# Performance work log

Measured on AMD Instinct MI355X. Metric: run time of the kernel, lower is better.

## Reference

```python
import jax, jax.numpy as jnp
from jax import lax
import numpy as np

B, C, L, H, W = 2, 64, 16, 64, 64
K = 7
NG = 4  # GroupNorm groups (SpatialGroupNorm(4, channels))


def setup_inputs() -> dict:
    key = jax.random.key(0)
    ks = jax.random.split(key, 16)
    s = lambda i, shape, sc: jax.random.normal(ks[i], shape, jnp.float32) * sc
    return {
        "x": s(0, (B, C, L, H, W), 1.0),
        "dt": jax.random.uniform(ks[1], (B, L), jnp.float32, 0.1, 1.0),
        "W_sp": s(2, (C, C, K, K), 0.02),      # spatial 7x7 conv (OIHW)
        "W_dc": s(3, (C, C), 0.1),             # 1x1x1 depth conv
        "b_dc": jnp.zeros((C,), jnp.float32),
        "gn_g": jnp.ones((C,), jnp.float32),
        "gn_b": jnp.zeros((C,), jnp.float32),
        "W_in": s(4, (2 * C, C), 0.1),         # pw_conv_in 1x1 -> 2C (gated)
        "b_in": jnp.zeros((2 * C,), jnp.float32),
        "W_out": s(5, (C, C), 0.1),            # pw_conv_out 1x1
        "b_out": jnp.zeros((C,), jnp.float32),
        "nu_log": s(6, (C,), 0.5),             # LRU log decay rate
        "theta_log": s(7, (C,), 0.5),          # LRU log frequency
        "c_re": s(8, (C,), 0.5),               # LRU output mix (real)
        "c_im": s(9, (C,), 0.5),               # LRU output mix (imag)
        "d_skip": s(10, (C,), 0.5),            # LRU feedthrough
    }


def reference(x, dt, W_sp, W_dc, b_dc, gn_g, gn_b, W_in, b_in, W_out, b_out,
              nu_log, theta_log, c_re, c_im, d_skip):
    Bb, Cc, Ll, Hh, Ww = x.shape
    pad = W_sp.shape[-1] // 2
    # --- GatedConvBlock: FactorizedPeriodicConv3d (per-frame 2D conv) ---
    xf = x.transpose(0, 2, 1, 3, 4).reshape(Bb * Ll, Cc, Hh, Ww)  # [B*L,C,H,W]
    xp = jnp.pad(xf, ((0, 0), (0, 0), (0, 0), (pad, pad)), mode='wrap')    # circular W
    xp = jnp.pad(xp, ((0, 0), (0, 0), (pad, pad), (0, 0)), mode='edge')    # replicate H
    y = lax.conv_general_dilated(xp, W_sp, (1, 1), 'VALID',
                                 dimension_numbers=('NCHW', 'OIHW', 'NCHW'))
    y = jnp.einsum('nchw,oc->nohw', y, W_dc) + b_dc[None, :, None, None]   # depth 1x1x1
    # --- SpatialGroupNorm (per frame, 4 groups) ---
    g = y.reshape(Bb * Ll, NG, Cc // NG, Hh, Ww)
    mu = g.mean(axis=(2, 3, 4), keepdims=True)
    var = g.var(axis=(2, 3, 4), keepdims=True)
    y = ((g - mu) * lax.rsqrt(var + 1e-5)).reshape(Bb * Ll, Cc, Hh, Ww)
    y = y * gn_g[None, :, None, None] + gn_b[None, :, None, None]
    # --- gated pointwise convs + residual ---
    h = jnp.einsum('nchw,oc->nohw', y, W_in) + b_in[None, :, None, None]
    x1, x2 = jnp.split(h, 2, axis=1)
    z = x1 * jax.nn.sigmoid(x2)
    z = jnp.einsum('nchw,oc->nohw', z, W_out) + b_out[None, :, None, None]
    u = xf + z                                     # residual, [B*L,C,H,W]
    u = u.reshape(Bb, Ll, Cc, Hh, Ww).transpose(1, 0, 2, 3, 4)  # [L,B,C,H,W]
    # --- LRU: dt-dependent complex diagonal recurrence over L ---
    decay = jnp.exp(-jnp.exp(nu_log)[None, None, :] * dt[:, :, None])   # [B,L,C]
    phase = jnp.exp(theta_log)[None, None, :] * dt[:, :, None]          # [B,L,C]
    lam_re = (decay * jnp.cos(phase)).transpose(1, 0, 2)[..., None, None]  # [L,B,C,1,1]
    lam_im = (decay * jnp.sin(phase)).transpose(1, 0, 2)[..., None, None]
    gamma = jnp.sqrt(jnp.maximum(1.0 - decay ** 2, 1e-6)).transpose(1, 0, 2)[..., None, None]
    cr = c_re[None, :, None, None]
    ci = c_im[None, :, None, None]
    ds = d_skip[None, :, None, None]

    def step(carry, inputs):
        h_re, h_im = carry
        ut, lr, li, gm = inputs
        nr = lr * h_re - li * h_im + gm * ut
        ni = li * h_re + lr * h_im
        yt = cr * nr + ci * ni + ds * ut
        return (nr, ni), yt

    init = (jnp.zeros((Bb, Cc, Hh, Ww), x.dtype), jnp.zeros((Bb, Cc, Hh, Ww), x.dtype))
    _, ys = lax.scan(step, init, (u, lam_re, lam_im, gamma))   # ys: [L,B,C,H,W]
    return ys.transpose(1, 2, 0, 3, 4)                         # [B,C,L,H,W]
```

## Files before the change

### kernel.cpp

```cpp
#include <hip/hip_runtime.h>
#include <hip/hip_bf16.h>

typedef short bf16x8 __attribute__((ext_vector_type(8)));
typedef float f32x16 __attribute__((ext_vector_type(16)));

#define B_ 2
#define C_ 64
#define L_ 16
#define N_ 32
#define HW_ 4096

#define BY_WPH  0u
#define BY_WP1  401408u
#define BY_WP2  434176u
#define BY_OFF1 450560u
#define BY_LR   451072u
#define BY_LI   459264u
#define BY_GM   467456u
#define BY_PART 475648u
#define BY_XHI  524288u
#define BY_U    524288u

__device__ __forceinline__ unsigned short f2bf(float v) {
    unsigned int u = __float_as_uint(v);
    unsigned int r = u + 0x7FFFu + ((u >> 16) & 1u);
    return (unsigned short)(r >> 16);
}
__device__ __forceinline__ float bf2f(unsigned short s) {
    return __uint_as_float(((unsigned int)s) << 16);
}

__global__ void k_setup(const float* __restrict__ W_sp, const float* __restrict__ W_dc,
                        unsigned short* __restrict__ WpH,
                        const float* __restrict__ W_in, const float* __restrict__ b_in,
                        const float* __restrict__ W_out,
                        const float* __restrict__ gn_g, const float* __restrict__ gn_b,
                        unsigned short* __restrict__ WP1, unsigned short* __restrict__ WP2,
                        float* __restrict__ OFF1,
                        const float* __restrict__ dt, const float* __restrict__ nu_log,
                        const float* __restrict__ theta_log,
                        float* __restrict__ lr_t, float* __restrict__ li_t,
                        float* __restrict__ gm_t) {
    int blk = blockIdx.x, tid = threadIdx.x;
    if (blk < 98) {
        int idx = blk * 256 + tid;
        if (idx >= 49 * 512) return;
        int lane = idx & 63;
        int ks   = (idx >> 6) & 3;
        int nf   = (idx >> 8) & 1;
        int tap  = idx >> 9;
        int oc   = nf * 32 + (lane & 31);
        int icb  = ks * 16 + (lane >> 5) * 8;
        unsigned short h8[8];
        #pragma unroll
        for (int e = 0; e < 8; ++e) {
            int ic = icb + e;
            float s = 0.f;
            for (int c = 0; c < 64; ++c)
                s += W_dc[oc * 64 + c] * W_sp[(c * 64 + ic) * 49 + tap];
            h8[e] = f2bf(s);
        }
        #pragma unroll
        for (int e = 0; e < 8; ++e) WpH[idx * 8 + e] = h8[e];
    } else if (blk < 111) {
        int idx = (blk - 98) * 256 + tid;
        if (idx < 2048) {
            int lane = idx & 63, ks = (idx >> 6) & 3, nf = (idx >> 8) & 3, hl = idx >> 10;
            int o = nf * 32 + (lane & 31), cb = ks * 16 + (lane >> 5) * 8;
            #pragma unroll
            for (int e = 0; e < 8; ++e) {
                float v = W_in[o * 64 + cb + e] * gn_g[cb + e];
                unsigned short h = f2bf(v);
                WP1[idx * 8 + e] = hl ? f2bf(v - bf2f(h)) : h;
            }
        } else if (idx < 3072) {
            int i2 = idx - 2048;
            int lane = i2 & 63, ks = (i2 >> 6) & 3, nf = (i2 >> 8) & 1, hl = i2 >> 9;
            int j = nf * 32 + (lane & 31), ob = ks * 16 + (lane >> 5) * 8;
            #pragma unroll
            for (int e = 0; e < 8; ++e) {
                float v = W_out[j * 64 + ob + e];
                unsigned short h = f2bf(v);
                WP2[i2 * 8 + e] = hl ? f2bf(v - bf2f(h)) : h;
            }
        } else if (idx < 3200) {
            int o = idx - 3072;
            float s = b_in[o];
            for (int c = 0; c < 64; ++c) s += W_in[o * 64 + c] * gn_b[c];
            OFF1[o] = s;
        }
    } else {
        int idx = (blk - 111) * 256 + tid;
        if (idx >= N_ * C_) return;
        int c = idx & 63, n = idx >> 6;
        float dtv = dt[n];
        float decay = expf(-expf(nu_log[c]) * dtv);
        float phase = expf(theta_log[c]) * dtv;
        lr_t[idx] = decay * cosf(phase);
        li_t[idx] = decay * sinf(phase);
        gm_t[idx] = sqrtf(fmaxf(1.f - decay * decay, 1e-6f));
    }
}

__global__ __launch_bounds__(256) void k_tr(const float* __restrict__ x,
                                            unsigned short* __restrict__ xhi) {
    __shared__ float t[64][129];
    int blk = blockIdx.x;
    int n = blk >> 5, seg = blk & 31;
    int p0 = seg * 128;
    int b = n >> 4, l = n & 15;
    int tid = threadIdx.x;
    for (int i = 0; i < 32; ++i) {
        int idx = i * 256 + tid;
        int ic = idx >> 7, p = idx & 127;
        t[ic][p] = x[(((size_t)(b * 64 + ic) * 16 + l)) * 4096 + p0 + p];
    }
    __syncthreads();
    for (int it = 0; it < 4; ++it) {
        int chunk = it * 256 + tid;
        int p = chunk >> 3, c0 = (chunk & 7) * 8;
        unsigned short h8[8];
        #pragma unroll
        for (int e = 0; e < 8; ++e) h8[e] = f2bf(t[c0 + e][p]);
        size_t off = ((size_t)(n * 4096 + p0 + p)) * 64 + c0;
        *(uint4*)&xhi[off] = *(uint4*)h8;
    }
}

__global__ __launch_bounds__(256, 2) void k_conv(
    const unsigned short* __restrict__ xhi,
    const unsigned short* __restrict__ WpH,
    const float* __restrict__ b_dc, unsigned short* __restrict__ y,
    float* __restrict__ part) {
    __shared__ uint4 halo[3904];
    __shared__ float ps[4][8], pq[4][8];
    int tid = threadIdx.x;
    int tile = blockIdx.x;
    int th = tile >> 2, tw = tile & 3;
    int n = blockIdx.y;
    int lane = tid & 63, wid = tid >> 6;
    int dh = (lane >> 4) & 1, dw = lane & 15, kslot = lane >> 5;

    for (int u2 = wid; u2 < 61; u2 += 4) {
        int row = u2 * 8 + (lane >> 3);
        if (row > 483) row = 483;
        int hh = row / 22, ww = row - hh * 22;
        int hs = th * 16 + hh - 3; hs = hs < 0 ? 0 : (hs > 63 ? 63 : hs);
        int wv = (tw * 16 + ww - 3) & 63;
        const uint4* src = (const uint4*)(xhi + ((size_t)n * 4096 + hs * 64 + wv) * 64) + (lane & 7);
        uint4 v = *src;
        *(uint4*)((char*)halo + ((row << 7) + (((lane & 7) ^ (row & 7)) << 4))) = v;
    }
    __syncthreads();

    f32x16 acc[2][2] = {};
    bf16x8 Aa[2][4], Ab[2][4], Ba[2][4], Bb[2][4];

#define LOADA(Areg, khv, kwv) { \
    _Pragma("unroll") for (int m = 0; m < 2; ++m) { \
        int rowb = (wid * 4 + 2 * m + dh + (khv)) * 22 + dw + (kwv); \
        _Pragma("unroll") for (int ks = 0; ks < 4; ++ks) { \
            int byt = (rowb << 7) + (((2 * ks + kslot) ^ (rowb & 7)) << 4); \
            Areg[m][ks] = *(const bf16x8*)((const char*)halo + byt); } } }

#define LOADB(Breg, tap) { \
    const bf16x8* WH = (const bf16x8*)WpH + (size_t)(tap) * 512 + lane; \
    _Pragma("unroll") for (int nf = 0; nf < 2; ++nf) \
        _Pragma("unroll") for (int ks = 0; ks < 4; ++ks) \
            Breg[nf][ks] = WH[(nf * 4 + ks) * 64]; }

#define MFMA_ALL(Areg, Breg) { \
    _Pragma("unroll") for (int ks = 0; ks < 4; ++ks) \
        _Pragma("unroll") for (int m = 0; m < 2; ++m) \
            _Pragma("unroll") for (int nf = 0; nf < 2; ++nf) \
                acc[m][nf] = __builtin_amdgcn_mfma_f32_32x32x16_bf16(Areg[m][ks], Breg[nf][ks], acc[m][nf], 0, 0, 0); }

    int kh = 0, kw = 0;
    LOADA(Aa, 0, 0); LOADB(Ba, 0);
    for (int t = 0; t < 48; t += 2) {
        ++kw; if (kw == 7) { kw = 0; ++kh; }
        LOADA(Ab, kh, kw);
        MFMA_ALL(Aa, Ba);
        LOADB(Bb, t + 1);
        ++kw; if (kw == 7) { kw = 0; ++kh; }
        LOADA(Aa, kh, kw);
        MFMA_ALL(Ab, Bb);
        LOADB(Ba, t + 2);
    }
    MFMA_ALL(Aa, Ba);
#undef LOADA
#undef LOADB
#undef MFMA_ALL

    int ocl = lane & 31;
    float sg[2], qg[2];
    #pragma unroll
    for (int nf = 0; nf < 2; ++nf) {
        float bv = b_dc[nf * 32 + ocl];
        float ss = 0.f, qq = 0.f;
        #pragma unroll
        for (int m = 0; m < 2; ++m) {
            #pragma unroll
            for (int j = 0; j < 16; ++j) {
                int r = (j & 3) + 8 * (j >> 2) + 4 * (lane >> 5);
                int h = th * 16 + wid * 4 + 2 * m + (r >> 4);
                int w = tw * 16 + (r & 15);
                float v = acc[m][nf][j] + bv;
                y[((size_t)n * 4096 + h * 64 + w) * 64 + nf * 32 + ocl] = f2bf(v);
                ss += v; qq += v * v;
            }
        }
        sg[nf] = ss; qg[nf] = qq;
    }
    #pragma unroll
    for (int off = 1; off < 16; off <<= 1) {
        sg[0] += __shfl_xor(sg[0], off);
        qg[0] += __shfl_xor(qg[0], off);
        sg[1] += __shfl_xor(sg[1], off);
        qg[1] += __shfl_xor(qg[1], off);
    }
    if ((lane & 15) == 0) {
        int cl = lane >> 4;
        int g0 = cl & 1, slot = wid * 2 + (cl >> 1);
        ps[g0][slot] = sg[0];     pq[g0][slot] = qg[0];
        ps[2 + g0][slot] = sg[1]; pq[2 + g0][slot] = qg[1];
    }
    __syncthreads();
    if (tid < 4) {
        float ss = 0.f, qq = 0.f;
        #pragma unroll
        for (int k2 = 0; k2 < 8; ++k2) { ss += ps[tid][k2]; qq += pq[tid][k2]; }
        part[((size_t)(n * 16 + tile)) * 8 + tid * 2]     = ss;
        part[((size_t)(n * 16 + tile)) * 8 + tid * 2 + 1] = qq;
    }
}

__global__ __launch_bounds__(256, 1) void k_pw(
    const unsigned short* __restrict__ y, const float* __restrict__ part,
    const unsigned short* __restrict__ WP1, const unsigned short* __restrict__ WP2,
    const float* __restrict__ OFF1, const float* __restrict__ b_out,
    const float* __restrict__ x, float* __restrict__ u) {
    __shared__ __align__(16) char lds[4 * 8704];
    int tid = threadIdx.x, lane = tid & 63, wid = tid >> 6;
    int blk = blockIdx.x;
    int n = blk >> 5, sub = blk & 31;
    int b = n >> 4, l = n & 15;
    int ocl = lane & 31, hi5 = lane >> 5;
    int pixw = sub * 128 + wid * 32;
    char* myl = lds + wid * 8704;

    float mu[4], rsd[4];
    #pragma unroll
    for (int g = 0; g < 4; ++g) {
        float sm = 0.f, sq = 0.f;
        #pragma unroll
        for (int ch = 0; ch < 16; ++ch) {
            sm += part[(n * 16 + ch) * 8 + g * 2];
            sq += part[(n * 16 + ch) * 8 + g * 2 + 1];
        }
        float mean = sm * (1.f / 65536.f);
        float var  = sq * (1.f / 65536.f) - mean * mean;
        mu[g] = mean;
        rsd[g] = rsqrtf(var + 1e-5f);
    }

    const bf16x8* W1 = (const bf16x8*)WP1;
    const bf16x8* W2 = (const bf16x8*)WP2;

    int prow = pixw + ocl;

    bf16x8 A1[4];
    #pragma unroll
    for (int ks = 0; ks < 4; ++ks) {
        bf16x8 raw = *(const bf16x8*)&y[(size_t)(n * 4096 + prow) * 64 + ks * 16 + hi5 * 8];
        float m = mu[ks], r = rsd[ks];
        bf16x8 a;
        #pragma unroll
        for (int e = 0; e < 8; ++e)
            a[e] = (short)f2bf((bf2f((unsigned short)raw[e]) - m) * r);
        A1[ks] = a;
    }

    f32x16 acc1[4];
    #pragma unroll
    for (int nf = 0; nf < 4; ++nf) {
        float o0 = OFF1[nf * 32 + ocl];
        #pragma unroll
        for (int j = 0; j < 16; ++j) acc1[nf][j] = o0;
    }
    __builtin_amdgcn_s_setprio(1);
    #pragma unroll
    for (int ks = 0; ks < 4; ++ks)
        #pragma unroll
        for (int nf = 0; nf < 4; ++nf) {
            bf16x8 bh = W1[nf * 256 + ks * 64 + lane];
            bf16x8 bl = W1[1024 + nf * 256 + ks * 64 + lane];
            acc1[nf] = __builtin_amdgcn_mfma_f32_32x32x16_bf16(A1[ks], bh, acc1[nf], 0, 0, 0);
            acc1[nf] = __builtin_amdgcn_mfma_f32_32x32x16_bf16(A1[ks], bl, acc1[nf], 0, 0, 0);
        }
    __builtin_amdgcn_s_setprio(0);

    unsigned short* zp = (unsigned short*)myl;
    #pragma unroll
    for (int nf = 0; nf < 2; ++nf)
        #pragma unroll
        for (int j = 0; j < 16; ++j) {
            int r = (j & 3) + 8 * (j >> 2) + 4 * hi5;
            float x1 = acc1[nf][j], x2 = acc1[nf + 2][j];
            float z = x1 / (1.f + __expf(-x2));
            zp[r * 68 + nf * 32 + ocl] = f2bf(z);
        }
    asm volatile("s_waitcnt lgkmcnt(0)" ::: "memory");
    __builtin_amdgcn_sched_barrier(0);

    bf16x8 A2[4];
    #pragma unroll
    for (int ks = 0; ks < 4; ++ks)
        A2[ks] = *(const bf16x8*)(myl + ocl * 136 + ks * 32 + hi5 * 16);

    f32x16 acc2[2];
    #pragma unroll
    for (int nf = 0; nf < 2; ++nf)
        #pragma unroll
        for (int j = 0; j < 16; ++j) acc2[nf][j] = 0.f;
    __builtin_amdgcn_s_setprio(1);
    #pragma unroll
    for (int ks = 0; ks < 4; ++ks)
        #pragma unroll
        for (int nf = 0; nf < 2; ++nf) {
            bf16x8 bh = W2[nf * 256 + ks * 64 + lane];
            bf16x8 bl = W2[512 + nf * 256 + ks * 64 + lane];
            acc2[nf] = __builtin_amdgcn_mfma_f32_32x32x16_bf16(A2[ks], bh, acc2[nf], 0, 0, 0);
            acc2[nf] = __builtin_amdgcn_mfma_f32_32x32x16_bf16(A2[ks], bl, acc2[nf], 0, 0, 0);
        }
    __builtin_amdgcn_s_setprio(0);
    asm volatile("s_waitcnt lgkmcnt(0)" ::: "memory");
    __builtin_amdgcn_sched_barrier(0);

    float* up = (float*)myl;
    #pragma unroll
    for (int nf = 0; nf < 2; ++nf)
        #pragma unroll
        for (int j = 0; j < 16; ++j) {
            int r = (j & 3) + 8 * (j >> 2) + 4 * hi5;
            up[r * 68 + nf * 32 + ocl] = acc2[nf][j];
        }
    asm volatile("s_waitcnt lgkmcnt(0)" ::: "memory");
    __builtin_amdgcn_sched_barrier(0);

    {
        float* rowp = up + ocl * 68 + hi5 * 32;
        float vrow[32];
        #pragma unroll
        for (int c4 = 0; c4 < 8; ++c4) {
            float4 v = *(const float4*)&rowp[c4 * 4];
            vrow[c4 * 4 + 0] = v.x; vrow[c4 * 4 + 1] = v.y;
            vrow[c4 * 4 + 2] = v.z; vrow[c4 * 4 + 3] = v.w;
        }
        int pixg = pixw + ocl;
        #pragma unroll
        for (int k = 0; k < 32; ++k) {
            int c = hi5 * 32 + k;
            vrow[k] += b_out[c] + x[((size_t)(b * 64 + c) * 16 + l) * 4096 + pixg];
        }
        #pragma unroll
        for (int c4 = 0; c4 < 8; ++c4) {
            float4 v;
            v.x = vrow[c4 * 4 + 0]; v.y = vrow[c4 * 4 + 1];
            v.z = vrow[c4 * 4 + 2]; v.w = vrow[c4 * 4 + 3];
            *(float4*)&rowp[c4 * 4] = v;
        }
    }
    asm volatile("s_waitcnt lgkmcnt(0)" ::: "memory");
    __builtin_amdgcn_sched_barrier(0);

    #pragma unroll
    for (int i = 0; i < 8; ++i) {
        int e = i * 64 + lane;
        int row = e >> 4, c4 = e & 15;
        float4 v = *(const float4*)&up[row * 68 + c4 * 4];
        *(float4*)&u[((size_t)(n * 4096 + pixw + row)) * 64 + c4 * 4] = v;
    }
    asm volatile("s_waitcnt lgkmcnt(0)" ::: "memory");
    __builtin_amdgcn_sched_barrier(0);
}

__global__ __launch_bounds__(256) void k_scan(
    const float* __restrict__ u, const float* __restrict__ lr_t,
    const float* __restrict__ li_t, const float* __restrict__ gm_t,
    const float* __restrict__ c_re, const float* __restrict__ c_im,
    const float* __restrict__ d_skip, float* __restrict__ out) {
    __shared__ float us[2][16][36];
    int tid = threadIdx.x;
    int bid = blockIdx.x;
    int b = bid >> 9, h = (bid >> 3) & 63, wq = (bid >> 1) & 3, ch = bid & 1;
    int c2 = tid & 15, p = tid >> 4;
    int w = wq * 16 + p;
    int cbase = ch * 32 + c2 * 2;
    float2 cr2 = *(const float2*)&c_re[cbase];
    float2 ci2 = *(const float2*)&c_im[cbase];
    float2 ds2 = *(const float2*)&d_skip[cbase];
    float hr0 = 0.f, hi0 = 0.f, hr1 = 0.f, hi1 = 0.f;
    int wp = tid & 15, cc = tid >> 4;
    size_t ubase = ((size_t)(b * 16) * 4096 + h * 64 + w) * 64 + cbase;
    int lbase = (b * 16) * 64 + cbase;
    float2 uv  = *(const float2*)&u[ubase];
    float2 lr2 = *(const float2*)&lr_t[lbase];
    float2 li2 = *(const float2*)&li_t[lbase];
    float2 gm2 = *(const float2*)&gm_t[lbase];
    for (int l = 0; l < 16; ++l) {
        float2 uvn, lrn, lin, gmn;
        if (l < 15) {
            uvn = *(const float2*)&u[ubase + (size_t)(l + 1) * 262144];
            lrn = *(const float2*)&lr_t[lbase + (l + 1) * 64];
            lin = *(const float2*)&li_t[lbase + (l + 1) * 64];
            gmn = *(const float2*)&gm_t[lbase + (l + 1) * 64];
        }
        float nr0 = lr2.x * hr0 - li2.x * hi0 + gm2.x * uv.x;
        float ni0 = li2.x * hr0 + lr2.x * hi0;
        float y0  = cr2.x * nr0 + ci2.x * ni0 + ds2.x * uv.x; hr0 = nr0; hi0 = ni0;
        float nr1 = lr2.y * hr1 - li2.y * hi1 + gm2.y * uv.y;
        float ni1 = li2.y * hr1 + lr2.y * hi1;
        float y1  = cr2.y * nr1 + ci2.y * ni1 + ds2.y * uv.y; hr1 = nr1; hi1 = ni1;
        float2 st; st.x = y0; st.y = y1;
        *(float2*)&us[l & 1][p][c2 * 2] = st;
        __syncthreads();
        out[((size_t)(b * 64 + ch * 32 + cc * 2)     * 16 + l) * 4096 + h * 64 + wq * 16 + wp] = us[l & 1][wp][cc * 2];
        out[((size_t)(b * 64 + ch * 32 + cc * 2 + 1) * 16 + l) * 4096 + h * 64 + wq * 16 + wp] = us[l & 1][wp][cc * 2 + 1];
        uv = uvn; lr2 = lrn; li2 = lin; gm2 = gmn;
    }
}

extern "C" void kernel_launch(void* const* d_in, const int* in_sizes, int n_in,
                              void* d_out, int out_size, void* d_ws, size_t ws_size,
                              hipStream_t stream) {
    const float* x        = (const float*)d_in[0];
    const float* dt       = (const float*)d_in[1];
    const float* W_sp     = (const float*)d_in[2];
    const float* W_dc     = (const float*)d_in[3];
    const float* b_dc     = (const float*)d_in[4];
    const float* gn_g     = (const float*)d_in[5];
    const float* gn_b     = (const float*)d_in[6];
    const float* W_in     = (const float*)d_in[7];
    const float* b_in     = (const float*)d_in[8];
    const float* W_out    = (const float*)d_in[9];
    const float* b_out    = (const float*)d_in[10];
    const float* nu_log   = (const float*)d_in[11];
    const float* theta_log= (const float*)d_in[12];
    const float* c_re     = (const float*)d_in[13];
    const float* c_im     = (const float*)d_in[14];
    const float* d_skip   = (const float*)d_in[15];

    char* ws = (char*)d_ws;
    unsigned short* WpH  = (unsigned short*)(ws + BY_WPH);
    unsigned short* WP1  = (unsigned short*)(ws + BY_WP1);
    unsigned short* WP2  = (unsigned short*)(ws + BY_WP2);
    float* OFF1   = (float*)(ws + BY_OFF1);
    float* lr_t   = (float*)(ws + BY_LR);
    float* li_t   = (float*)(ws + BY_LI);
    float* gm_t   = (float*)(ws + BY_GM);
    float* part   = (float*)(ws + BY_PART);
    unsigned short* xhi = (unsigned short*)(ws + BY_XHI);
    float* u      = (float*)(ws + BY_U);
    unsigned short* y16 = (unsigned short*)d_out;
    float* out    = (float*)d_out;

    hipLaunchKernelGGL(k_setup,   dim3(119),       dim3(256), 0, stream,
                       W_sp, W_dc, WpH, W_in, b_in, W_out, gn_g, gn_b, WP1, WP2, OFF1,
                       dt, nu_log, theta_log, lr_t, li_t, gm_t);
    hipLaunchKernelGGL(k_tr,      dim3(1024),      dim3(256), 0, stream, x, xhi);
    hipLaunchKernelGGL(k_conv,    dim3(16, 32),    dim3(256), 0, stream, xhi, WpH, b_dc, y16, part);
    hipLaunchKernelGGL(k_pw,      dim3(1024),      dim3(256), 0, stream, y16, part, WP1, WP2,
                       OFF1, b_out, x, u);
    hipLaunchKernelGGL(k_scan,    dim3(1024),      dim3(256), 0, stream, u, lr_t, li_t, gm_t,
                       c_re, c_im, d_skip, out);
}
```

Before: 129.4 us.

## Store pointwise output as bf16 in place over transposed input buffer

The pointwise kernel now reads the residual from the bf16 channel-last copy of x (xhi) rather than the strided fp32 x, and writes the intermediate u back into the same buffer in bf16. It also drops the LDS round trip and the separate coalesced store. The scan kernel reads bf16 pairs instead of float2. This halves the intermediate traffic and removes a strided fp32 gather. The cost is precision: the residual and u are rounded to bf16 before the recurrence.

```diff
diff --git a/kernel.cpp b/kernel.cpp
--- a/kernel.cpp
+++ b/kernel.cpp
@@ -19,7 +19,6 @@
 #define BY_GM   467456u
 #define BY_PART 475648u
 #define BY_XHI  524288u
-#define BY_U    524288u
 
 __device__ __forceinline__ unsigned short f2bf(float v) {
     unsigned int u = __float_as_uint(v);
@@ -239,12 +238,11 @@
     const unsigned short* __restrict__ y, const float* __restrict__ part,
     const unsigned short* __restrict__ WP1, const unsigned short* __restrict__ WP2,
     const float* __restrict__ OFF1, const float* __restrict__ b_out,
-    const float* __restrict__ x, float* __restrict__ u) {
+    unsigned short* __restrict__ xr ) {
     __shared__ __align__(16) char lds[4 * 8704];
     int tid = threadIdx.x, lane = tid & 63, wid = tid >> 6;
     int blk = blockIdx.x;
     int n = blk >> 5, sub = blk & 31;
-    int b = n >> 4, l = n & 15;
     int ocl = lane & 31, hi5 = lane >> 5;
     int pixw = sub * 128 + wid * 32;
     char* myl = lds + wid * 8704;
@@ -349,7 +347,7 @@
     __builtin_amdgcn_sched_barrier(0);
 
     {
-        float* rowp = up + ocl * 68 + hi5 * 32;
+        const float* rowp = up + ocl * 68 + hi5 * 32;
         float vrow[32];
         #pragma unroll
         for (int c4 = 0; c4 < 8; ++c4) {
@@ -358,35 +356,30 @@
             vrow[c4 * 4 + 2] = v.z; vrow[c4 * 4 + 3] = v.w;
         }
         int pixg = pixw + ocl;
-        #pragma unroll
-        for (int k = 0; k < 32; ++k) {
-            int c = hi5 * 32 + k;
-            vrow[k] += b_out[c] + x[((size_t)(b * 64 + c) * 16 + l) * 4096 + pixg];
-        }
-        #pragma unroll
-        for (int c4 = 0; c4 < 8; ++c4) {
-            float4 v;
-            v.x = vrow[c4 * 4 + 0]; v.y = vrow[c4 * 4 + 1];
-            v.z = vrow[c4 * 4 + 2]; v.w = vrow[c4 * 4 + 3];
-            *(float4*)&rowp[c4 * 4] = v;
-        }
+        unsigned short* xrow = &xr[((size_t)(n * 4096 + pixg)) * 64 + hi5 * 32];
+        bf16x8 xv0 = *(const bf16x8*)&xrow[0];
+        bf16x8 xv1 = *(const bf16x8*)&xrow[8];
+        bf16x8 xv2 = *(const bf16x8*)&xrow[16];
+        bf16x8 xv3 = *(const bf16x8*)&xrow[24];
+        unsigned short h16[32];
+        #pragma unroll
+        for (int e = 0; e < 8; ++e) {
+            h16[e]      = f2bf(vrow[e]      + b_out[hi5 * 32 + e]      + bf2f((unsigned short)xv0[e]));
+            h16[8 + e]  = f2bf(vrow[8 + e]  + b_out[hi5 * 32 + 8 + e]  + bf2f((unsigned short)xv1[e]));
+            h16[16 + e] = f2bf(vrow[16 + e] + b_out[hi5 * 32 + 16 + e] + bf2f((unsigned short)xv2[e]));
+            h16[24 + e] = f2bf(vrow[24 + e] + b_out[hi5 * 32 + 24 + e] + bf2f((unsigned short)xv3[e]));
+        }
+        *(uint4*)&xrow[0]  = *(uint4*)&h16[0];
+        *(uint4*)&xrow[8]  = *(uint4*)&h16[8];
+        *(uint4*)&xrow[16] = *(uint4*)&h16[16];
+        *(uint4*)&xrow[24] = *(uint4*)&h16[24];
     }
     asm volatile("s_waitcnt lgkmcnt(0)" ::: "memory");
     __builtin_amdgcn_sched_barrier(0);
-
-    #pragma unroll
-    for (int i = 0; i < 8; ++i) {
-        int e = i * 64 + lane;
-        int row = e >> 4, c4 = e & 15;
-        float4 v = *(const float4*)&up[row * 68 + c4 * 4];
-        *(float4*)&u[((size_t)(n * 4096 + pixw + row)) * 64 + c4 * 4] = v;
-    }
-    asm volatile("s_waitcnt lgkmcnt(0)" ::: "memory");
-    __builtin_amdgcn_sched_barrier(0);
 }
 
 __global__ __launch_bounds__(256) void k_scan(
-    const float* __restrict__ u, const float* __restrict__ lr_t,
+    const unsigned short* __restrict__ u16, const float* __restrict__ lr_t,
     const float* __restrict__ li_t, const float* __restrict__ gm_t,
     const float* __restrict__ c_re, const float* __restrict__ c_im,
     const float* __restrict__ d_skip, float* __restrict__ out) {
@@ -404,30 +397,33 @@
     int wp = tid & 15, cc = tid >> 4;
     size_t ubase = ((size_t)(b * 16) * 4096 + h * 64 + w) * 64 + cbase;
     int lbase = (b * 16) * 64 + cbase;
-    float2 uv  = *(const float2*)&u[ubase];
+    unsigned int uraw = *(const unsigned int*)&u16[ubase];
     float2 lr2 = *(const float2*)&lr_t[lbase];
     float2 li2 = *(const float2*)&li_t[lbase];
     float2 gm2 = *(const float2*)&gm_t[lbase];
     for (int l = 0; l < 16; ++l) {
-        float2 uvn, lrn, lin, gmn;
+        unsigned int urawn = 0;
+        float2 lrn, lin, gmn;
         if (l < 15) {
-            uvn = *(const float2*)&u[ubase + (size_t)(l + 1) * 262144];
+            urawn = *(const unsigned int*)&u16[ubase + (size_t)(l + 1) * 262144];
             lrn = *(const float2*)&lr_t[lbase + (l + 1) * 64];
             lin = *(const float2*)&li_t[lbase + (l + 1) * 64];
             gmn = *(const float2*)&gm_t[lbase + (l + 1) * 64];
         }
-        float nr0 = lr2.x * hr0 - li2.x * hi0 + gm2.x * uv.x;
+        float ux = bf2f((unsigned short)(uraw & 0xffff));
+        float uy = bf2f((unsigned short)(uraw >> 16));
+        float nr0 = lr2.x * hr0 - li2.x * hi0 + gm2.x * ux;
         float ni0 = li2.x * hr0 + lr2.x * hi0;
-        float y0  = cr2.x * nr0 + ci2.x * ni0 + ds2.x * uv.x; hr0 = nr0; hi0 = ni0;
-        float nr1 = lr2.y * hr1 - li2.y * hi1 + gm2.y * uv.y;
+        float y0  = cr2.x * nr0 + ci2.x * ni0 + ds2.x * ux; hr0 = nr0; hi0 = ni0;
+        float nr1 = lr2.y * hr1 - li2.y * hi1 + gm2.y * uy;
         float ni1 = li2.y * hr1 + lr2.y * hi1;
-        float y1  = cr2.y * nr1 + ci2.y * ni1 + ds2.y * uv.y; hr1 = nr1; hi1 = ni1;
+        float y1  = cr2.y * nr1 + ci2.y * ni1 + ds2.y * uy; hr1 = nr1; hi1 = ni1;
         float2 st; st.x = y0; st.y = y1;
         *(float2*)&us[l & 1][p][c2 * 2] = st;
         __syncthreads();
         out[((size_t)(b * 64 + ch * 32 + cc * 2)     * 16 + l) * 4096 + h * 64 + wq * 16 + wp] = us[l & 1][wp][cc * 2];
         out[((size_t)(b * 64 + ch * 32 + cc * 2 + 1) * 16 + l) * 4096 + h * 64 + wq * 16 + wp] = us[l & 1][wp][cc * 2 + 1];
-        uv = uvn; lr2 = lrn; li2 = lin; gm2 = gmn;
+        uraw = urawn; lr2 = lrn; li2 = lin; gm2 = gmn;
     }
 }
 
@@ -461,7 +457,6 @@
     float* gm_t   = (float*)(ws + BY_GM);
     float* part   = (float*)(ws + BY_PART);
     unsigned short* xhi = (unsigned short*)(ws + BY_XHI);
-    float* u      = (float*)(ws + BY_U);
     unsigned short* y16 = (unsigned short*)d_out;
     float* out    = (float*)d_out;
 
@@ -471,7 +466,7 @@
     hipLaunchKernelGGL(k_tr,      dim3(1024),      dim3(256), 0, stream, x, xhi);
     hipLaunchKernelGGL(k_conv,    dim3(16, 32),    dim3(256), 0, stream, xhi, WpH, b_dc, y16, part);
     hipLaunchKernelGGL(k_pw,      dim3(1024),      dim3(256), 0, stream, y16, part, WP1, WP2,
-                       OFF1, b_out, x, u);
-    hipLaunchKernelGGL(k_scan,    dim3(1024),      dim3(256), 0, stream, u, lr_t, li_t, gm_t,
+                       OFF1, b_out, xhi);
+    hipLaunchKernelGGL(k_scan,    dim3(1024),      dim3(256), 0, stream, xhi, lr_t, li_t, gm_t,
                        c_re, c_im, d_skip, out);
 }
```

Result: no change. 126.8 us (-2.0%).
